# Kernel optimization log

Measured on AMD Instinct MI355X. Metric: run time of the kernel, lower is better.

Reference implementation:

```python
import jax, jax.numpy as jnp
import numpy as np
from jax import lax

TAU_MEM = 20.0
DT = 1.0
NOISE_STD = 0.05
INHIBITION = 0.1
V_THRESH = 1.0
CUE_STRENGTH = 1.0

N_NEURONS = 2048
BATCH = 128
STEPS = 200
CUE_DURATION = 10
SPARSITY = 0.1


def setup_inputs() -> dict:
    key = jax.random.key(0)
    k1, k2, k3 = jax.random.split(key, 3)
    cue = (jax.random.uniform(k1, (BATCH, N_NEURONS)) < SPARSITY).astype(jnp.float32)
    weights = jax.random.normal(k2, (N_NEURONS, N_NEURONS), dtype=jnp.float32) * 0.01
    # pre-drawn per-step membrane noise (replaces LIF internal RNG, deterministic)
    noise = jax.random.normal(k3, (STEPS, BATCH, N_NEURONS), dtype=jnp.float32) * NOISE_STD
    return {"cue": cue, "weights": weights, "noise": noise,
            "steps": STEPS, "cue_duration": CUE_DURATION}


def reference(cue, weights, noise, steps, cue_duration):
    n = weights.shape[0]
    dtype = weights.dtype
    # effective weights: mask self-connections, add global inhibition -inh/n
    self_mask = (1.0 - jnp.eye(n, dtype=dtype))
    w_eff = (weights - INHIBITION / n) * self_mask  # [n, n]

    decay = jnp.asarray(np.exp(-DT / TAU_MEM), dtype=dtype)
    half = steps // 2

    zeros = jnp.zeros_like(cue)

    def step(carry, xs):
        mem, last_spk, acc = carry
        t, nz = xs
        # recurrent input from previous spikes (zero on first step, as in torch)
        rec = last_spk @ w_eff                                   # [B, n]
        ext = jnp.where(t < cue_duration, CUE_STRENGTH, 0.0) * cue
        total = rec + ext
        # LIF update: leak, integrate, noise
        mem = mem * decay + total + nz
        spk = (mem >= V_THRESH).astype(dtype)
        mem = mem * (1.0 - spk)                                  # hard reset
        # accumulate activity over second half of simulation
        acc = acc + jnp.where(t >= half, 1.0, 0.0) * spk
        return (mem, spk, acc), None

    ts = jnp.arange(steps)
    (_, _, acc), _ = lax.scan(step, (zeros, zeros, zeros), (ts, noise))
    mean_activity = acc / half                                   # [B, n]
    return mean_activity
```

## Files before the change

kernel.cpp:

```cpp
#include <hip/hip_runtime.h>


typedef float        f32x4 __attribute__((ext_vector_type(4)));
typedef unsigned int u32x4 __attribute__((ext_vector_type(4)));

constexpr int N   = 2048;
constexpr int PT  = 4;
constexpr int BLK = N / PT;

__device__ __forceinline__ f32x4 ntload4(const float* p) {
    return __builtin_nontemporal_load(reinterpret_cast<const f32x4*>(p));
}

__global__ __launch_bounds__(BLK)
void attractor_sim(const float* __restrict__ cue,
                   const float* __restrict__ W,
                   const float* __restrict__ noise,
                   const int*   __restrict__ steps_p,
                   const int*   __restrict__ cuedur_p,
                   float*       __restrict__ out,
                   int batch)
{
    const int b    = blockIdx.x;
    const int tid  = threadIdx.x;
    const int base = tid * PT;

    __shared__ __align__(16) unsigned short lst[3][N];
    __shared__ int cnt[3];
    if (tid < 3) cnt[tid] = 0;

    const int   steps  = *steps_p;
    const int   cuedur = *cuedur_p;
    const int   half   = steps / 2;
    const float decay  = 0.95122942450071400910f;
    const float C_INH  = 0.1f / 2048.0f;

    const f32x4 ce = *reinterpret_cast<const f32x4*>(cue + (size_t)b * N + base);

    float wdiag[PT];
    #pragma unroll
    for (int u = 0; u < PT; ++u)
        wdiag[u] = W[(size_t)(base + u) * N + (base + u)];

    f32x4 mem = {0.f, 0.f, 0.f, 0.f};
    f32x4 acc = {0.f, 0.f, 0.f, 0.f};
    unsigned lastspk = 0;

    const size_t stepstride = (size_t)batch * N;
    const float* nzp = noise + (size_t)b * N + base;

    f32x4 n0 = ntload4(nzp);
    f32x4 n1 = ntload4(nzp + (size_t)(steps > 1 ? 1 : 0) * stepstride);
    f32x4 n2;

    __syncthreads();

    auto body = [&](int t, f32x4& nUse, f32x4& nFill, int ra, int wb, int rc) {
        const int tpre = (t + 2 < steps) ? (t + 2) : (steps - 1);
        nFill = ntload4(nzp + (size_t)tpre * stepstride);

        const int k = cnt[ra];
        if (tid == 0) cnt[rc] = 0;
        const unsigned short* lp = lst[ra];

        f32x4 r = {0.f, 0.f, 0.f, 0.f};
        int i = 0;
        for (; i + 8 <= k; i += 8) {
            const u32x4 iv = *reinterpret_cast<const u32x4*>(lp + i);
            const int j0 = (int)(iv[0] & 0xffffu), j1 = (int)(iv[0] >> 16);
            const int j2 = (int)(iv[1] & 0xffffu), j3 = (int)(iv[1] >> 16);
            const int j4 = (int)(iv[2] & 0xffffu), j5 = (int)(iv[2] >> 16);
            const int j6 = (int)(iv[3] & 0xffffu), j7 = (int)(iv[3] >> 16);
            const f32x4 w0 = *reinterpret_cast<const f32x4*>(W + j0 * N + base);
            const f32x4 w1 = *reinterpret_cast<const f32x4*>(W + j1 * N + base);
            const f32x4 w2 = *reinterpret_cast<const f32x4*>(W + j2 * N + base);
            const f32x4 w3 = *reinterpret_cast<const f32x4*>(W + j3 * N + base);
            const f32x4 w4 = *reinterpret_cast<const f32x4*>(W + j4 * N + base);
            const f32x4 w5 = *reinterpret_cast<const f32x4*>(W + j5 * N + base);
            const f32x4 w6 = *reinterpret_cast<const f32x4*>(W + j6 * N + base);
            const f32x4 w7 = *reinterpret_cast<const f32x4*>(W + j7 * N + base);
            r += w0; r += w1; r += w2; r += w3;
            r += w4; r += w5; r += w6; r += w7;
        }
        for (; i < k; ++i) {
            const int j = lp[i];
            r += *reinterpret_cast<const f32x4*>(W + j * N + base);
        }

        const float corr   = (float)k * C_INH;
        const bool  in_cue = (t < cuedur);

        unsigned newspk = 0;
        #pragma unroll
        for (int u = 0; u < PT; ++u) {
            float rec = r[u] - corr;
            if (lastspk & (1u << u)) rec -= (wdiag[u] - C_INH);
            const float ext = in_cue ? ce[u] : 0.0f;
            const float m   = mem[u] * decay + (rec + ext) + nUse[u];
            if (m >= 1.0f) {
                mem[u] = 0.0f;
                newspk |= (1u << u);
                const int pos = atomicAdd(&cnt[wb], 1);
                lst[wb][pos] = (unsigned short)(base + u);
                if (t >= half) acc[u] += 1.0f;
            } else {
                mem[u] = m;
            }
        }
        lastspk = newspk;

        __syncthreads();
    };

    int t = 0;
    for (; t + 3 <= steps; t += 3) {
        body(t,     n0, n2, 0, 1, 2);
        body(t + 1, n1, n0, 1, 2, 0);
        body(t + 2, n2, n1, 2, 0, 1);
    }
    for (; t < steps; ++t) {
        switch (t % 3) {
            case 0: body(t, n0, n2, 0, 1, 2); break;
            case 1: body(t, n1, n0, 1, 2, 0); break;
            default: body(t, n2, n1, 2, 0, 1); break;
        }
    }

    const float h = (float)half;
    f32x4 o;
    o[0] = acc[0] / h; o[1] = acc[1] / h; o[2] = acc[2] / h; o[3] = acc[3] / h;
    float* op = out + (size_t)b * N + base;
    __builtin_nontemporal_store(o, reinterpret_cast<f32x4*>(op));
}

extern "C" void kernel_launch(void* const* d_in, const int* in_sizes, int n_in,
                              void* d_out, int out_size, void* d_ws, size_t ws_size,
                              hipStream_t stream) {
    const float* cue    = (const float*)d_in[0];
    const float* W      = (const float*)d_in[1];
    const float* noise  = (const float*)d_in[2];
    const int*   steps  = (const int*)d_in[3];
    const int*   cuedur = (const int*)d_in[4];
    float*       out    = (float*)d_out;

    const int batch = in_sizes[0] / N;
    attractor_sim<<<batch, BLK, 0, stream>>>(cue, W, noise, steps, cuedur, out, batch);
}
```

Baseline: 524.2 us.

## Gather recurrent weights from a bf16 copy and compact spikes with wave ballots

Adds a pre-pass that converts the weight matrix to bf16 in the workspace, so the per-step sparse row gathers read half the bytes. Per-spike LDS atomics are replaced by a wave ballot, one atomic per wave and popcount offsets, and the noise prefetch depth grows from two steps ahead to four. The bf16 weights add rounding to the recurrent sums, which can flip threshold crossings and so change spike counts. A small conversion kernel now runs on every call.

Result: faster. 497.7 us (-5.1%).

```diff
diff --git a/kernel.cpp b/kernel.cpp
--- a/kernel.cpp
+++ b/kernel.cpp
@@ -1,8 +1,10 @@
 #include <hip/hip_runtime.h>
 
 
-typedef float        f32x4 __attribute__((ext_vector_type(4)));
-typedef unsigned int u32x4 __attribute__((ext_vector_type(4)));
+typedef float          f32x4 __attribute__((ext_vector_type(4)));
+typedef unsigned int   u32x4 __attribute__((ext_vector_type(4)));
+typedef unsigned int   u32x2 __attribute__((ext_vector_type(2)));
+typedef unsigned short u16x8 __attribute__((ext_vector_type(8)));
 
 constexpr int N   = 2048;
 constexpr int PT  = 4;
@@ -11,10 +13,40 @@
 __device__ __forceinline__ f32x4 ntload4(const float* p) {
     return __builtin_nontemporal_load(reinterpret_cast<const f32x4*>(p));
 }
-
+__device__ __forceinline__ float bf2f(unsigned b) {
+    return __builtin_bit_cast(float, b << 16);
+}
+__device__ __forceinline__ void addrow_bf(f32x4& r, u32x2 v) {
+    r[0] += __builtin_bit_cast(float, v[0] << 16);
+    r[1] += __builtin_bit_cast(float, v[0] & 0xffff0000u);
+    r[2] += __builtin_bit_cast(float, v[1] << 16);
+    r[3] += __builtin_bit_cast(float, v[1] & 0xffff0000u);
+}
+
+__global__ __launch_bounds__(256)
+void conv_bf16(const float* __restrict__ W, unsigned short* __restrict__ Wb) {
+    const size_t i = ((size_t)blockIdx.x * 256 + threadIdx.x) * 8;
+    const f32x4 a = *reinterpret_cast<const f32x4*>(W + i);
+    const f32x4 b = *reinterpret_cast<const f32x4*>(W + i + 4);
+    u16x8 o;
+    #pragma unroll
+    for (int u = 0; u < 4; ++u) {
+        const unsigned x = __builtin_bit_cast(unsigned, a[u]);
+        o[u] = (unsigned short)((x + 0x7fffu + ((x >> 16) & 1u)) >> 16);
+    }
+    #pragma unroll
+    for (int u = 0; u < 4; ++u) {
+        const unsigned x = __builtin_bit_cast(unsigned, b[u]);
+        o[4 + u] = (unsigned short)((x + 0x7fffu + ((x >> 16) & 1u)) >> 16);
+    }
+    *reinterpret_cast<u16x8*>(Wb + i) = o;
+}
+
+template <int WM>
 __global__ __launch_bounds__(BLK)
 void attractor_sim(const float* __restrict__ cue,
                    const float* __restrict__ W,
+                   const unsigned short* __restrict__ Wb,
                    const float* __restrict__ noise,
                    const int*   __restrict__ steps_p,
                    const int*   __restrict__ cuedur_p,
@@ -24,6 +56,7 @@
     const int b    = blockIdx.x;
     const int tid  = threadIdx.x;
     const int base = tid * PT;
+    const int lane = tid & 63;
 
     __shared__ __align__(16) unsigned short lst[3][N];
     __shared__ int cnt[3];
@@ -39,25 +72,31 @@
 
     float wdiag[PT];
     #pragma unroll
-    for (int u = 0; u < PT; ++u)
-        wdiag[u] = W[(size_t)(base + u) * N + (base + u)];
+    for (int u = 0; u < PT; ++u) {
+        const size_t d = (size_t)(base + u) * N + (base + u);
+        wdiag[u] = (WM == 1) ? bf2f((unsigned)Wb[d]) : W[d];
+    }
 
     f32x4 mem = {0.f, 0.f, 0.f, 0.f};
     f32x4 acc = {0.f, 0.f, 0.f, 0.f};
     unsigned lastspk = 0;
 
-    const size_t stepstride = (size_t)batch * N;
+    const size_t ss  = (size_t)batch * N;
     const float* nzp = noise + (size_t)b * N + base;
 
-    f32x4 n0 = ntload4(nzp);
-    f32x4 n1 = ntload4(nzp + (size_t)(steps > 1 ? 1 : 0) * stepstride);
-    f32x4 n2;
+    f32x4 n0 = ntload4(nzp + (size_t)((0 < steps) ? 0 : steps - 1) * ss);
+    f32x4 n1 = ntload4(nzp + (size_t)((1 < steps) ? 1 : steps - 1) * ss);
+    f32x4 n2 = ntload4(nzp + (size_t)((2 < steps) ? 2 : steps - 1) * ss);
+    f32x4 n3 = ntload4(nzp + (size_t)((3 < steps) ? 3 : steps - 1) * ss);
+
+    int ra = 0, wb = 1, rc = 2;
 
     __syncthreads();
 
-    auto body = [&](int t, f32x4& nUse, f32x4& nFill, int ra, int wb, int rc) {
-        const int tpre = (t + 2 < steps) ? (t + 2) : (steps - 1);
-        nFill = ntload4(nzp + (size_t)tpre * stepstride);
+    auto body = [&](int t, f32x4& nReg) {
+        const f32x4 cur = nReg;
+        const int tp = (t + 4 < steps) ? (t + 4) : (steps - 1);
+        nReg = ntload4(nzp + (size_t)tp * ss);
 
         const int k = cnt[ra];
         if (tid == 0) cnt[rc] = 0;
@@ -65,43 +104,65 @@
 
         f32x4 r = {0.f, 0.f, 0.f, 0.f};
         int i = 0;
-        for (; i + 8 <= k; i += 8) {
-            const u32x4 iv = *reinterpret_cast<const u32x4*>(lp + i);
-            const int j0 = (int)(iv[0] & 0xffffu), j1 = (int)(iv[0] >> 16);
-            const int j2 = (int)(iv[1] & 0xffffu), j3 = (int)(iv[1] >> 16);
-            const int j4 = (int)(iv[2] & 0xffffu), j5 = (int)(iv[2] >> 16);
-            const int j6 = (int)(iv[3] & 0xffffu), j7 = (int)(iv[3] >> 16);
-            const f32x4 w0 = *reinterpret_cast<const f32x4*>(W + j0 * N + base);
-            const f32x4 w1 = *reinterpret_cast<const f32x4*>(W + j1 * N + base);
-            const f32x4 w2 = *reinterpret_cast<const f32x4*>(W + j2 * N + base);
-            const f32x4 w3 = *reinterpret_cast<const f32x4*>(W + j3 * N + base);
-            const f32x4 w4 = *reinterpret_cast<const f32x4*>(W + j4 * N + base);
-            const f32x4 w5 = *reinterpret_cast<const f32x4*>(W + j5 * N + base);
-            const f32x4 w6 = *reinterpret_cast<const f32x4*>(W + j6 * N + base);
-            const f32x4 w7 = *reinterpret_cast<const f32x4*>(W + j7 * N + base);
-            r += w0; r += w1; r += w2; r += w3;
-            r += w4; r += w5; r += w6; r += w7;
-        }
-        for (; i < k; ++i) {
-            const int j = lp[i];
-            r += *reinterpret_cast<const f32x4*>(W + j * N + base);
+        if (WM == 1) {
+            for (; i + 8 <= k; i += 8) {
+                const u32x4 iv = *reinterpret_cast<const u32x4*>(lp + i);
+                const int j0 = (int)(iv[0] & 0xffffu), j1 = (int)(iv[0] >> 16);
+                const int j2 = (int)(iv[1] & 0xffffu), j3 = (int)(iv[1] >> 16);
+                const int j4 = (int)(iv[2] & 0xffffu), j5 = (int)(iv[2] >> 16);
+                const int j6 = (int)(iv[3] & 0xffffu), j7 = (int)(iv[3] >> 16);
+                const u32x2 v0 = *reinterpret_cast<const u32x2*>(Wb + (size_t)j0 * N + base);
+                const u32x2 v1 = *reinterpret_cast<const u32x2*>(Wb + (size_t)j1 * N + base);
+                const u32x2 v2 = *reinterpret_cast<const u32x2*>(Wb + (size_t)j2 * N + base);
+                const u32x2 v3 = *reinterpret_cast<const u32x2*>(Wb + (size_t)j3 * N + base);
+                const u32x2 v4 = *reinterpret_cast<const u32x2*>(Wb + (size_t)j4 * N + base);
+                const u32x2 v5 = *reinterpret_cast<const u32x2*>(Wb + (size_t)j5 * N + base);
+                const u32x2 v6 = *reinterpret_cast<const u32x2*>(Wb + (size_t)j6 * N + base);
+                const u32x2 v7 = *reinterpret_cast<const u32x2*>(Wb + (size_t)j7 * N + base);
+                addrow_bf(r, v0); addrow_bf(r, v1); addrow_bf(r, v2); addrow_bf(r, v3);
+                addrow_bf(r, v4); addrow_bf(r, v5); addrow_bf(r, v6); addrow_bf(r, v7);
+            }
+            for (; i < k; ++i) {
+                const u32x2 v = *reinterpret_cast<const u32x2*>(Wb + (size_t)lp[i] * N + base);
+                addrow_bf(r, v);
+            }
+        } else {
+            for (; i + 8 <= k; i += 8) {
+                const u32x4 iv = *reinterpret_cast<const u32x4*>(lp + i);
+                const int j0 = (int)(iv[0] & 0xffffu), j1 = (int)(iv[0] >> 16);
+                const int j2 = (int)(iv[1] & 0xffffu), j3 = (int)(iv[1] >> 16);
+                const int j4 = (int)(iv[2] & 0xffffu), j5 = (int)(iv[2] >> 16);
+                const int j6 = (int)(iv[3] & 0xffffu), j7 = (int)(iv[3] >> 16);
+                const f32x4 w0 = *reinterpret_cast<const f32x4*>(W + (size_t)j0 * N + base);
+                const f32x4 w1 = *reinterpret_cast<const f32x4*>(W + (size_t)j1 * N + base);
+                const f32x4 w2 = *reinterpret_cast<const f32x4*>(W + (size_t)j2 * N + base);
+                const f32x4 w3 = *reinterpret_cast<const f32x4*>(W + (size_t)j3 * N + base);
+                const f32x4 w4 = *reinterpret_cast<const f32x4*>(W + (size_t)j4 * N + base);
+                const f32x4 w5 = *reinterpret_cast<const f32x4*>(W + (size_t)j5 * N + base);
+                const f32x4 w6 = *reinterpret_cast<const f32x4*>(W + (size_t)j6 * N + base);
+                const f32x4 w7 = *reinterpret_cast<const f32x4*>(W + (size_t)j7 * N + base);
+                r += w0; r += w1; r += w2; r += w3;
+                r += w4; r += w5; r += w6; r += w7;
+            }
+            for (; i < k; ++i)
+                r += *reinterpret_cast<const f32x4*>(W + (size_t)lp[i] * N + base);
         }
 
         const float corr   = (float)k * C_INH;
         const bool  in_cue = (t < cuedur);
 
         unsigned newspk = 0;
+        bool sp[PT];
         #pragma unroll
         for (int u = 0; u < PT; ++u) {
             float rec = r[u] - corr;
             if (lastspk & (1u << u)) rec -= (wdiag[u] - C_INH);
             const float ext = in_cue ? ce[u] : 0.0f;
-            const float m   = mem[u] * decay + (rec + ext) + nUse[u];
-            if (m >= 1.0f) {
+            const float m   = mem[u] * decay + (rec + ext) + cur[u];
+            sp[u] = (m >= 1.0f);
+            if (sp[u]) {
                 mem[u] = 0.0f;
                 newspk |= (1u << u);
-                const int pos = atomicAdd(&cnt[wb], 1);
-                lst[wb][pos] = (unsigned short)(base + u);
                 if (t >= half) acc[u] += 1.0f;
             } else {
                 mem[u] = m;
@@ -109,28 +170,44 @@
         }
         lastspk = newspk;
 
+        #pragma unroll
+        for (int u = 0; u < PT; ++u) {
+            const unsigned long long msk = __ballot(sp[u]);
+            if (msk) {
+                int wpos;
+                if (lane == 0) wpos = atomicAdd(&cnt[wb], __popcll(msk));
+                wpos = __shfl(wpos, 0);
+                if (sp[u]) {
+                    const int off = __popcll(msk & ((1ull << lane) - 1ull));
+                    lst[wb][wpos + off] = (unsigned short)(base + u);
+                }
+            }
+        }
+
         __syncthreads();
+        const int t0 = ra; ra = wb; wb = rc; rc = t0;
     };
 
     int t = 0;
-    for (; t + 3 <= steps; t += 3) {
-        body(t,     n0, n2, 0, 1, 2);
-        body(t + 1, n1, n0, 1, 2, 0);
-        body(t + 2, n2, n1, 2, 0, 1);
+    for (; t + 4 <= steps; t += 4) {
+        body(t,     n0);
+        body(t + 1, n1);
+        body(t + 2, n2);
+        body(t + 3, n3);
     }
     for (; t < steps; ++t) {
-        switch (t % 3) {
-            case 0: body(t, n0, n2, 0, 1, 2); break;
-            case 1: body(t, n1, n0, 1, 2, 0); break;
-            default: body(t, n2, n1, 2, 0, 1); break;
+        switch (t & 3) {
+            case 0:  body(t, n0); break;
+            case 1:  body(t, n1); break;
+            case 2:  body(t, n2); break;
+            default: body(t, n3); break;
         }
     }
 
     const float h = (float)half;
     f32x4 o;
     o[0] = acc[0] / h; o[1] = acc[1] / h; o[2] = acc[2] / h; o[3] = acc[3] / h;
-    float* op = out + (size_t)b * N + base;
-    __builtin_nontemporal_store(o, reinterpret_cast<f32x4*>(op));
+    __builtin_nontemporal_store(o, reinterpret_cast<f32x4*>(out + (size_t)b * N + base));
 }
 
 extern "C" void kernel_launch(void* const* d_in, const int* in_sizes, int n_in,
@@ -144,5 +221,13 @@
     float*       out    = (float*)d_out;
 
     const int batch = in_sizes[0] / N;
-    attractor_sim<<<batch, BLK, 0, stream>>>(cue, W, noise, steps, cuedur, out, batch);
-}
+    const size_t need = (size_t)N * N * 2;
+
+    if (ws_size >= need) {
+        unsigned short* Wb = (unsigned short*)d_ws;
+        conv_bf16<<<(N * N) / (256 * 8), 256, 0, stream>>>(W, Wb);
+        attractor_sim<1><<<batch, BLK, 0, stream>>>(cue, W, Wb, noise, steps, cuedur, out, batch);
+    } else {
+        attractor_sim<0><<<batch, BLK, 0, stream>>>(cue, W, nullptr, noise, steps, cuedur, out, batch);
+    }
+}
```
